# Kernel optimization log

Hardware: AMD Instinct MI355X
Metric: run time of the kernel (lower is better)

The kernel has to match this reference:

```python
import math
import jax, jax.numpy as jnp
import numpy as np

B, S, HID = 2, 1024, 2048
H, D, R = 16, 128, 64            # heads, head_dim, rope_dim_per_head
KVC, QC = 512, 1536              # kv / query compressed dims
MAX_POS = 4096


def _lin(x, w, b):
    return x @ w.T + b


def _rotate_half(x):
    x1, x2 = x[..., : x.shape[-1] // 2], x[..., x.shape[-1] // 2 :]
    return jnp.concatenate([-x2, x1], axis=-1)


def _rope_tables(dim, end, theta=10000.0):
    freqs = 1.0 / (theta ** (jnp.arange(0, dim, 2)[: dim // 2].astype(jnp.float32) / dim))
    f = jnp.outer(jnp.arange(end, dtype=jnp.float32), freqs)  # [end, dim//2]
    cos, sin = jnp.cos(f), jnp.sin(f)
    # duplicate halves so tables broadcast against the full rope dim (standard HF convention)
    return jnp.concatenate([cos, cos], -1), jnp.concatenate([sin, sin], -1)


def setup_inputs() -> dict:
    key = jax.random.key(0)
    ks = jax.random.split(key, 17)
    w = lambda k, shape: (jax.random.normal(k, shape, jnp.float32) * 0.02)
    return {
        "hidden_states": jax.random.normal(ks[0], (B, S, HID), jnp.float32),
        "W_DKV_w": w(ks[1], (KVC, HID)),  "W_DKV_b": w(ks[2], (KVC,)),
        "W_UK_w":  w(ks[3], (H * D, KVC)), "W_UK_b":  w(ks[4], (H * D,)),
        "W_UV_w":  w(ks[5], (H * D, KVC)), "W_UV_b":  w(ks[6], (H * D,)),
        "W_KR_w":  w(ks[7], (R, D)),       "W_KR_b":  w(ks[8], (R,)),
        "W_DQ_w":  w(ks[9], (QC, HID)),    "W_DQ_b":  w(ks[10], (QC,)),
        "W_UQ_w":  w(ks[11], (H * D, QC)), "W_UQ_b":  w(ks[12], (H * D,)),
        "W_QR_w":  w(ks[13], (R, D)),      "W_QR_b":  w(ks[14], (R,)),
        "W_O_w":   w(ks[15], (HID, H * D)),"W_O_b":   w(ks[16], (HID,)),
    }


def reference(hidden_states, W_DKV_w, W_DKV_b, W_UK_w, W_UK_b, W_UV_w, W_UV_b,
              W_KR_w, W_KR_b, W_DQ_w, W_DQ_b, W_UQ_w, W_UQ_b,
              W_QR_w, W_QR_b, W_O_w, W_O_b):
    b, s = hidden_states.shape[:2]
    # latent KV compression + decompression
    c_kv = _lin(hidden_states, W_DKV_w, W_DKV_b)                      # [B,S,KVC]
    k = _lin(c_kv, W_UK_w, W_UK_b).reshape(b, s, H, D)
    v = _lin(c_kv, W_UV_w, W_UV_b).reshape(b, s, H, D)
    # latent Q compression + decompression
    c_q = _lin(hidden_states, W_DQ_w, W_DQ_b)                         # [B,S,QC]
    q = _lin(c_q, W_UQ_w, W_UQ_b).reshape(b, s, H, D)
    # decoupled rope sub-dims
    k_r = _lin(k, W_KR_w, W_KR_b)                                     # [B,S,H,R]
    q_r = _lin(q, W_QR_w, W_QR_b)                                     # [B,S,H,R]
    cos, sin = _rope_tables(R, MAX_POS)
    cos_p = cos[:s][:, None, :]                                       # [S,1,R] -> broadcast over B,H
    sin_p = sin[:s][:, None, :]
    q_r = q_r * cos_p + _rotate_half(q_r) * sin_p
    k_r = k_r * cos_p + _rotate_half(k_r) * sin_p
    # SDPA (no mask, no causal flag in original)
    scale = 1.0 / math.sqrt(D)
    scores = jnp.einsum("bqhd,bkhd->bhqk", q, k) * scale              # [B,H,S,S]
    probs = jax.nn.softmax(scores, axis=-1)
    attn = jnp.einsum("bhqk,bkhd->bqhd", probs, v).reshape(b, s, H * D)
    output = _lin(attn, W_O_w, W_O_b)                                 # [B,S,HID]
    return output, c_kv, k_r
```

## Files before the change

### kernel.cpp

```cpp
#include <hip/hip_runtime.h>
#include <cstdint>

typedef __bf16 bf16;
typedef __attribute__((ext_vector_type(8))) __bf16 bf16x8;
typedef __attribute__((ext_vector_type(4))) float f32x4;

#define MFMA16(a, b, c) __builtin_amdgcn_mfma_f32_16x16x32_bf16(a, b, c, 0, 0, 0)

__device__ __forceinline__ void async16(const bf16* g, bf16* l) {
  __builtin_amdgcn_global_load_lds(
      (const __attribute__((address_space(1))) void*)g,
      (__attribute__((address_space(3))) void*)l, 16, 0, 0);
}

__device__ __forceinline__ bf16x8 load8cvt(const float* p) {
  f32x4 a = *(const f32x4*)p;
  f32x4 b = *(const f32x4*)(p + 4);
  bf16x8 r;
  r[0] = (bf16)a[0]; r[1] = (bf16)a[1]; r[2] = (bf16)a[2]; r[3] = (bf16)a[3];
  r[4] = (bf16)b[0]; r[5] = (bf16)b[1]; r[6] = (bf16)b[2]; r[7] = (bf16)b[3];
  return r;
}

__global__ __launch_bounds__(256) void cvt_f32_bf16(const float* __restrict__ src,
                                                    bf16* __restrict__ dst, int n) {
  int i = (blockIdx.x * 256 + threadIdx.x) * 8;
  if (i >= n) return;
  *(bf16x8*)(dst + i) = load8cvt(src + i);
}

__global__ __launch_bounds__(256) void cvt6(
    const float* __restrict__ s0, bf16* __restrict__ d0, int n0,
    const float* __restrict__ s1, bf16* __restrict__ d1, int n1,
    const float* __restrict__ s2, bf16* __restrict__ d2, int n2,
    const float* __restrict__ s3, bf16* __restrict__ d3, int n3,
    const float* __restrict__ s4, bf16* __restrict__ d4, int n4,
    const float* __restrict__ s5, bf16* __restrict__ d5, int n5) {
  const float* s; bf16* d; int n;
  switch (blockIdx.y) {
    case 0: s = s0; d = d0; n = n0; break;
    case 1: s = s1; d = d1; n = n1; break;
    case 2: s = s2; d = d2; n = n2; break;
    case 3: s = s3; d = d3; n = n3; break;
    case 4: s = s4; d = d4; n = n4; break;
    default: s = s5; d = d5; n = n5; break;
  }
  int i = (blockIdx.x * 256 + threadIdx.x) * 8;
  if (i >= n) return;
  *(bf16x8*)(d + i) = load8cvt(s + i);
}

template <int MODE>
__global__ __launch_bounds__(256) void gemm_bb(
    const bf16* __restrict__ A, int lda,
    const bf16* __restrict__ Bm, int ldb,
    const float* __restrict__ bias0, const float* __restrict__ bias1, int nsplit,
    bf16* __restrict__ outb, float* __restrict__ outf, int ldo,
    int M, int N, int K) {
  __shared__ __align__(16) bf16 As[2][128 * 32];
  __shared__ __align__(16) bf16 Bs[2][64 * 32];
  const int t = threadIdx.x;
  const int lane = t & 63, w = t >> 6;
  const int quad = lane >> 4, l15 = lane & 15;

  const int nwg = gridDim.x * gridDim.y;
  const int id = blockIdx.y * gridDim.x + blockIdx.x;
  const int sw = (id & 7) * (nwg >> 3) + (id >> 3);
  const int bm = (sw / gridDim.x) * 128, bn = (sw % gridDim.x) * 64;

  const int wm = (w >> 1) * 64, wn = (w & 1) * 32;

  f32x4 acc[4][2] = {};

  const int srow = t >> 2;
  const int scol = (t & 3) * 8;
  const bf16* Ap = A + (int64_t)(bm + srow) * lda + scol;
  const bf16* Bp = Bm + (int64_t)(bn + srow) * ldb + scol;

  auto STAGE = [&](int buf, int k0) {
    async16(Ap + k0, &As[buf][w * 512]);
    async16(Ap + (int64_t)64 * lda + k0, &As[buf][2048 + w * 512]);
    async16(Bp + k0, &Bs[buf][w * 512]);
  };
  auto COMPUTE = [&](int buf) {
    bf16x8 a[4], bq[2];
#pragma unroll
    for (int mt = 0; mt < 4; ++mt)
      a[mt] = *(const bf16x8*)(&As[buf][(wm + mt * 16 + l15) * 32 + quad * 8]);
#pragma unroll
    for (int nt = 0; nt < 2; ++nt)
      bq[nt] = *(const bf16x8*)(&Bs[buf][(wn + nt * 16 + l15) * 32 + quad * 8]);
#pragma unroll
    for (int mt = 0; mt < 4; ++mt)
#pragma unroll
      for (int nt = 0; nt < 2; ++nt)
        acc[mt][nt] = MFMA16(a[mt], bq[nt], acc[mt][nt]);
  };

  STAGE(0, 0);
  for (int k0 = 0; k0 < K; k0 += 64) {
    STAGE(1, k0 + 32);
    asm volatile("s_waitcnt vmcnt(3)\n\ts_barrier" ::: "memory");
    COMPUTE(0);
    asm volatile("s_waitcnt lgkmcnt(0)\n\ts_barrier" ::: "memory");
    if (k0 + 64 < K) {
      STAGE(0, k0 + 64);
      asm volatile("s_waitcnt vmcnt(3)\n\ts_barrier" ::: "memory");
    } else {
      asm volatile("s_waitcnt vmcnt(0)\n\ts_barrier" ::: "memory");
    }
    COMPUTE(1);
    asm volatile("s_waitcnt lgkmcnt(0)\n\ts_barrier" ::: "memory");
  }

  float bv[2];
#pragma unroll
  for (int nt = 0; nt < 2; ++nt) {
    int n = bn + wn + nt * 16 + l15;
    bv[nt] = (n < nsplit) ? bias0[n] : bias1[n - nsplit];
  }
#pragma unroll
  for (int mt = 0; mt < 4; ++mt)
#pragma unroll
    for (int nt = 0; nt < 2; ++nt)
#pragma unroll
      for (int r = 0; r < 4; ++r) {
        int64_t m = bm + wm + mt * 16 + quad * 4 + r;
        int n = bn + wn + nt * 16 + l15;
        float v = acc[mt][nt][r] + bv[nt];
        if (MODE != 1) outb[m * ldo + n] = (bf16)v;
        if (MODE == 1) outf[m * (int64_t)ldo + n] = v;
        if (MODE == 2 && n < nsplit) outf[m * nsplit + n] = v;
      }
}

__global__ __launch_bounds__(256) void kr_rope(const bf16* __restrict__ kmat,
                                               const float* __restrict__ Wkr,
                                               const float* __restrict__ bkr,
                                               float* __restrict__ krout) {
  const int t = threadIdx.x;
  const int lane = t & 63, w = t >> 6;
  const int quad = lane >> 4, l15 = lane & 15;
  const int row0 = blockIdx.x * 64 + w * 16;

  const int rr = row0 + l15;
  const bf16* krow = kmat + (int64_t)(rr >> 4) * 4096 + (rr & 15) * 128;
  bf16x8 af[4];
#pragma unroll
  for (int ks = 0; ks < 4; ++ks)
    af[ks] = *(const bf16x8*)(krow + ks * 32 + quad * 8);

  f32x4 acc[4] = {};
#pragma unroll
  for (int nt = 0; nt < 4; ++nt)
#pragma unroll
    for (int ks = 0; ks < 4; ++ks) {
      bf16x8 bf_ = load8cvt(Wkr + (nt * 16 + l15) * 128 + ks * 32 + quad * 8);
      acc[nt] = MFMA16(af[ks], bf_, acc[nt]);
    }

  float bv[4], fr[4];
#pragma unroll
  for (int nt = 0; nt < 4; ++nt) {
    bv[nt] = bkr[nt * 16 + l15];
    int j = ((nt & 1) * 16 + l15);
    fr[nt] = exp2f(-(float)j * 0.41524101186092034f);
  }

#pragma unroll
  for (int r = 0; r < 4; ++r) {
    int row = row0 + quad * 4 + r;
    int pos = (row >> 4) & 1023;
    float val[4];
#pragma unroll
    for (int nt = 0; nt < 4; ++nt) val[nt] = acc[nt][r] + bv[nt];
#pragma unroll
    for (int nt = 0; nt < 4; ++nt) {
      int n = nt * 16 + l15;
      float ang = (float)pos * fr[nt];
      float c = cosf(ang), s = sinf(ang);
      float partner = val[nt ^ 2];
      float o = val[nt] * c + ((nt < 2) ? -partner : partner) * s;
      krout[(int64_t)row * 64 + n] = o;
    }
  }
}

__global__ __launch_bounds__(512, 2) void attn_fwd(const bf16* __restrict__ q,
                                                   const bf16* __restrict__ k,
                                                   const bf16* __restrict__ v,
                                                   bf16* __restrict__ attn) {
  const int bh = blockIdx.x * 4 + (blockIdx.y >> 3);
  const int qt = blockIdx.y & 7;
  const int b = bh >> 4, h = bh & 15;
  __shared__ __align__(16) bf16 Vt[128 * 72];
  __shared__ __align__(16) bf16 Pl[8][16 * 72];

  const int t = threadIdx.x;
  const int lane = t & 63, w = t >> 6;
  const int quad = lane >> 4, l15 = lane & 15;
  const int trow = b * 1024 + qt * 128 + w * 16;
  const float scale = 0.08838834764831845f;

  bf16x8 qf[4];
#pragma unroll
  for (int ks = 0; ks < 4; ++ks)
    qf[ks] = *(const bf16x8*)(q + (int64_t)(trow + l15) * 2048 + h * 128 +
                              ks * 32 + quad * 8);

  const bf16* kbase = k + (int64_t)b * 1024 * 4096 + h * 128;

  const int skey = t >> 4;
  const int sd0 = (t & 15) * 8;
  const bf16* vp = v + (int64_t)b * 1024 * 4096 + h * 128 + sd0;

  bf16x8 vreg[2];
#pragma unroll
  for (int r = 0; r < 2; ++r)
    vreg[r] = *(const bf16x8*)(vp + (int64_t)(r * 32 + skey) * 4096);

  f32x4 o[8] = {};
  float lrow[4] = {0.f, 0.f, 0.f, 0.f};

  for (int kt = 0; kt < 16; ++kt) {
#pragma unroll
    for (int r = 0; r < 2; ++r) {
      int key = r * 32 + skey;
      int col = (((key >> 3) ^ ((sd0 >> 3) & 7)) << 3) + (key & 7);
#pragma unroll
      for (int j = 0; j < 8; ++j) Vt[(sd0 + j) * 72 + col] = vreg[r][j];
    }
    __syncthreads();

    if (kt + 1 < 16) {
#pragma unroll
      for (int r = 0; r < 2; ++r)
        vreg[r] = *(const bf16x8*)(vp + (int64_t)((kt + 1) * 64 + r * 32 + skey) * 4096);
    }

    const bf16* kp = kbase + (int64_t)kt * 64 * 4096;
    bf16x8 kf[16];
#pragma unroll
    for (int nt = 0; nt < 4; ++nt)
#pragma unroll
      for (int ks = 0; ks < 4; ++ks)
        kf[nt * 4 + ks] = *(const bf16x8*)(kp + (int64_t)(nt * 16 + l15) * 4096 +
                                           ks * 32 + quad * 8);
    f32x4 s[4] = {};
    __builtin_amdgcn_s_setprio(1);
#pragma unroll
    for (int nt = 0; nt < 4; ++nt)
#pragma unroll
      for (int ks = 0; ks < 4; ++ks)
        s[nt] = MFMA16(qf[ks], kf[nt * 4 + ks], s[nt]);
    __builtin_amdgcn_s_setprio(0);

    float rsum[4] = {0.f, 0.f, 0.f, 0.f};
#pragma unroll
    for (int nt = 0; nt < 4; ++nt)
#pragma unroll
      for (int r = 0; r < 4; ++r) {
        float p = __expf(s[nt][r] * scale);
        rsum[r] += p;
        int row = quad * 4 + r;
        int blk = (nt * 2 + (l15 >> 3)) ^ (quad * 2 + (r >> 1));
        Pl[w][row * 72 + (blk << 3) + (l15 & 7)] = (bf16)p;
      }
#pragma unroll
    for (int r = 0; r < 4; ++r) lrow[r] += rsum[r];

    __builtin_amdgcn_s_setprio(1);
#pragma unroll
    for (int ks = 0; ks < 2; ++ks) {
      int ablk = (ks * 4 + quad) ^ (l15 >> 1);
      bf16x8 afrg = *(const bf16x8*)(&Pl[w][l15 * 72 + (ablk << 3)]);
#pragma unroll
      for (int dt = 0; dt < 8; ++dt) {
        int d = dt * 16 + l15;
        int kb = ((ks * 4 + quad) ^ ((d >> 3) & 7)) << 3;
        bf16x8 bfrg = *(const bf16x8*)(Vt + d * 72 + kb);
        o[dt] = MFMA16(afrg, bfrg, o[dt]);
      }
    }
    __builtin_amdgcn_s_setprio(0);
    __syncthreads();
  }

  float inv[4];
#pragma unroll
  for (int r = 0; r < 4; ++r) {
    float ssum = lrow[r];
#pragma unroll
    for (int off = 8; off >= 1; off >>= 1) ssum += __shfl_xor(ssum, off, 64);
    inv[r] = 1.0f / ssum;
  }
#pragma unroll
  for (int dt = 0; dt < 8; ++dt)
#pragma unroll
    for (int r = 0; r < 4; ++r) {
      int64_t row = trow + quad * 4 + r;
      int col = h * 128 + dt * 16 + l15;
      attn[row * 2048 + col] = (bf16)(o[dt][r] * inv[r]);
    }
}

extern "C" void kernel_launch(void* const* d_in, const int* in_sizes, int n_in,
                              void* d_out, int out_size, void* d_ws, size_t ws_size,
                              hipStream_t stream) {
  const float* hidden = (const float*)d_in[0];
  const float* Wdkv = (const float*)d_in[1];
  const float* bdkv = (const float*)d_in[2];
  const float* Wuk  = (const float*)d_in[3];
  const float* buk  = (const float*)d_in[4];
  const float* Wuv  = (const float*)d_in[5];
  const float* buv  = (const float*)d_in[6];
  const float* Wkr  = (const float*)d_in[7];
  const float* bkr  = (const float*)d_in[8];
  const float* Wdq  = (const float*)d_in[9];
  const float* bdq  = (const float*)d_in[10];
  const float* Wuq  = (const float*)d_in[11];
  const float* buq  = (const float*)d_in[12];
  const float* Wo   = (const float*)d_in[15];
  const float* bo   = (const float*)d_in[16];

  float* out0 = (float*)d_out;
  float* c_kv = out0 + 4194304;
  float* k_r  = out0 + 5242880;

  bf16* DKVQ = (bf16*)d_ws;
  bf16* KV   = DKVQ + 4194304;

  bf16* WT   = KV;
  bf16* qx   = (bf16*)out0;
  bf16* hb   = qx + 4194304;
  bf16* WUKV = qx;
  bf16* Wuqb = hb;
  bf16* Wob  = (bf16*)k_r;

  cvt6<<<dim3(2048, 6), 256, 0, stream>>>(
      hidden, hb, 4194304,
      Wdkv, WT, 1048576,
      Wdq, WT + 1048576, 3145728,
      Wuk, WUKV, 1048576,
      Wuv, WUKV + 1048576, 1048576,
      Wo, Wob, 4194304);
  gemm_bb<2><<<dim3(32, 16), 256, 0, stream>>>(hb, 2048, WT, 2048, bdkv, bdq, 512,
                                               DKVQ, c_kv, 2048, 2048, 2048, 2048);
  cvt_f32_bf16<<<1536, 256, 0, stream>>>(Wuq, Wuqb, 3145728);
  gemm_bb<0><<<dim3(64, 16), 256, 0, stream>>>(DKVQ, 2048, WUKV, 512, buk, buv, 2048,
                                               KV, nullptr, 4096, 2048, 4096, 512);
  gemm_bb<0><<<dim3(32, 16), 256, 0, stream>>>(DKVQ + 512, 2048, Wuqb, 1536, buq, buq,
                                               2048, qx, nullptr, 2048, 2048, 2048, 1536);
  attn_fwd<<<dim3(8, 32), 512, 0, stream>>>(qx, KV, KV + 2048, DKVQ);
  gemm_bb<1><<<dim3(32, 16), 256, 0, stream>>>(DKVQ, 2048, Wob, 2048, bo, bo, 2048,
                                               nullptr, out0, 2048, 2048, 2048, 2048);
  kr_rope<<<512, 256, 0, stream>>>(KV, Wkr, bkr, k_r);
}
```

Baseline: 352.0 us.

## Stage K tiles in double-buffered LDS via async global-to-LDS loads

Each of the 8 waves in the attention kernel used to load the full 64x128 K tile from global memory into its own registers. Now the block loads each tile once, cooperatively, using global_load_lds into a swizzled, double-buffered LDS buffer. The next tile is prefetched while the current one is consumed, and the QK^T B-fragments are read from LDS. This cuts redundant global/L2 traffic and register pressure, at the cost of 32KB more LDS per block, which may limit occupancy. The end-of-iteration barrier is also replaced with an lgkmcnt wait plus s_barrier.

```diff
diff --git a/kernel.cpp b/kernel.cpp
--- a/kernel.cpp
+++ b/kernel.cpp
@@ -193,6 +193,7 @@
   const int bh = blockIdx.x * 4 + (blockIdx.y >> 3);
   const int qt = blockIdx.y & 7;
   const int b = bh >> 4, h = bh & 15;
+  __shared__ __align__(16) bf16 Kb[2][64 * 128];
   __shared__ __align__(16) bf16 Vt[128 * 72];
   __shared__ __align__(16) bf16 Pl[8][16 * 72];
 
@@ -209,20 +210,27 @@
                               ks * 32 + quad * 8);
 
   const bf16* kbase = k + (int64_t)b * 1024 * 4096 + h * 128;
+  const int lrow = lane >> 4;
+  const int64_t koff0 = (int64_t)(w * 8 + lrow) * 4096 + (((lane & 15) ^ lrow) << 3);
+  const int64_t koff1 = (int64_t)(w * 8 + 4 + lrow) * 4096 +
+                        (((lane & 15) ^ (4 + lrow)) << 3);
 
   const int skey = t >> 4;
   const int sd0 = (t & 15) * 8;
   const bf16* vp = v + (int64_t)b * 1024 * 4096 + h * 128 + sd0;
 
+  async16(kbase + koff0, &Kb[0][w * 1024]);
+  async16(kbase + koff1, &Kb[0][w * 1024 + 512]);
   bf16x8 vreg[2];
 #pragma unroll
   for (int r = 0; r < 2; ++r)
     vreg[r] = *(const bf16x8*)(vp + (int64_t)(r * 32 + skey) * 4096);
 
   f32x4 o[8] = {};
-  float lrow[4] = {0.f, 0.f, 0.f, 0.f};
+  float lrw[4] = {0.f, 0.f, 0.f, 0.f};
 
   for (int kt = 0; kt < 16; ++kt) {
+    const int cur = kt & 1;
 #pragma unroll
     for (int r = 0; r < 2; ++r) {
       int key = r * 32 + skey;
@@ -233,26 +241,25 @@
     __syncthreads();
 
     if (kt + 1 < 16) {
+      const bf16* kn = kbase + (int64_t)(kt + 1) * 64 * 4096;
+      async16(kn + koff0, &Kb[cur ^ 1][w * 1024]);
+      async16(kn + koff1, &Kb[cur ^ 1][w * 1024 + 512]);
 #pragma unroll
       for (int r = 0; r < 2; ++r)
         vreg[r] = *(const bf16x8*)(vp + (int64_t)((kt + 1) * 64 + r * 32 + skey) * 4096);
     }
 
-    const bf16* kp = kbase + (int64_t)kt * 64 * 4096;
-    bf16x8 kf[16];
-#pragma unroll
-    for (int nt = 0; nt < 4; ++nt)
-#pragma unroll
-      for (int ks = 0; ks < 4; ++ks)
-        kf[nt * 4 + ks] = *(const bf16x8*)(kp + (int64_t)(nt * 16 + l15) * 4096 +
-                                           ks * 32 + quad * 8);
     f32x4 s[4] = {};
     __builtin_amdgcn_s_setprio(1);
 #pragma unroll
     for (int nt = 0; nt < 4; ++nt)
 #pragma unroll
-      for (int ks = 0; ks < 4; ++ks)
-        s[nt] = MFMA16(qf[ks], kf[nt * 4 + ks], s[nt]);
+      for (int ks = 0; ks < 4; ++ks) {
+        int key = nt * 16 + l15;
+        bf16x8 bfrg = *(const bf16x8*)(
+            &Kb[cur][key * 128 + (((ks * 4 + quad) ^ (l15 & 7)) << 3)]);
+        s[nt] = MFMA16(qf[ks], bfrg, s[nt]);
+      }
     __builtin_amdgcn_s_setprio(0);
 
     float rsum[4] = {0.f, 0.f, 0.f, 0.f};
@@ -267,7 +274,7 @@
         Pl[w][row * 72 + (blk << 3) + (l15 & 7)] = (bf16)p;
       }
 #pragma unroll
-    for (int r = 0; r < 4; ++r) lrow[r] += rsum[r];
+    for (int r = 0; r < 4; ++r) lrw[r] += rsum[r];
 
     __builtin_amdgcn_s_setprio(1);
 #pragma unroll
@@ -283,13 +290,13 @@
       }
     }
     __builtin_amdgcn_s_setprio(0);
-    __syncthreads();
+    asm volatile("s_waitcnt lgkmcnt(0)\n\ts_barrier" ::: "memory");
   }
 
   float inv[4];
 #pragma unroll
   for (int r = 0; r < 4; ++r) {
-    float ssum = lrow[r];
+    float ssum = lrw[r];
 #pragma unroll
     for (int off = 8; off >= 1; off >>= 1) ssum += __shfl_xor(ssum, off, 64);
     inv[r] = 1.0f / ssum;
```

Result: faster. 312.1 us (-11.3%).
